# Kernel optimization log

Measured on AMD Instinct MI355X. Metric: run time of the kernel, lower is better.

The kernel has to match this reference:

```python
import jax, jax.numpy as jnp
import numpy as np

N_NODES = 200000
N_EDGES = 200000
X_SIZE = 256
H_SIZE = 256


def setup_inputs() -> dict:
    key = jax.random.key(0)
    ks = jax.random.split(key, 8)
    s = 1.0 / np.sqrt(H_SIZE)
    return {
        "x": jax.random.normal(ks[0], (N_NODES, X_SIZE), jnp.float32),
        "h": jax.random.normal(ks[1], (N_NODES, H_SIZE), jnp.float32),
        "c": jax.random.normal(ks[2], (N_NODES, H_SIZE), jnp.float32),
        "W_iou": jax.random.normal(ks[3], (3 * H_SIZE, X_SIZE), jnp.float32) * s,
        "U_iou": jax.random.normal(ks[4], (3 * H_SIZE, H_SIZE), jnp.float32) * s,
        "b_iou": jnp.zeros((1, 3 * H_SIZE), jnp.float32),
        "U_f_w": jax.random.normal(ks[5], (H_SIZE, H_SIZE), jnp.float32) * s,
        "U_f_b": jnp.zeros((H_SIZE,), jnp.float32),
        "edge_src": jax.random.randint(ks[6], (N_EDGES,), 0, N_NODES, jnp.int32),
        "edge_dst": jax.random.randint(ks[7], (N_EDGES,), 0, N_NODES, jnp.int32),
    }


def reference(x, h, c, W_iou, U_iou, b_iou, U_f_w, U_f_b, edge_src, edge_dst):
    n = x.shape[0]
    # --- message + reduce (DGL mailbox flattened to edge list) ---
    h_child = h[edge_src]                                   # [E, H] gather
    c_child = c[edge_src]                                   # [E, H]
    f = jax.nn.sigmoid(h_child @ U_f_w.T + U_f_b)           # per-child forget gate
    h_tild = jax.ops.segment_sum(h_child, edge_dst, num_segments=n)      # sum_j h_j
    c_agg = jax.ops.segment_sum(f * c_child, edge_dst, num_segments=n)   # sum_j f_j*c_j
    # --- node iou: W_iou(x) (node data) + U_iou(h_tild) from reduce ---
    iou = x @ W_iou.T + h_tild @ U_iou.T + b_iou            # [N, 3H]
    # --- apply_node_func ---
    i, o, u = jnp.split(iou, 3, axis=1)
    i = jax.nn.sigmoid(i)
    o = jax.nn.sigmoid(o)
    u = jnp.tanh(u)
    c_new = i * u + c_agg
    h_new = o * jnp.tanh(c_new)
    return h_new, c_new
```

## Files before the change

kernel.cpp:

```cpp
#include <hip/hip_runtime.h>

#define NN 200000
#define NE 200000
#define HD 256

typedef __attribute__((ext_vector_type(8))) short short8;
typedef __attribute__((ext_vector_type(4))) short short4v;
typedef __attribute__((ext_vector_type(4))) float f32x4;
typedef __attribute__((ext_vector_type(4))) unsigned int u32x4;

static __device__ __forceinline__ unsigned short f2bf(float f) {
  unsigned u = __float_as_uint(f);
  u = (u + 0x7FFFu + ((u >> 16) & 1u)) >> 16;
  return (unsigned short)u;
}
static __device__ __forceinline__ float bf2f(unsigned short u) {
  return __uint_as_float(((unsigned)u) << 16);
}
static __device__ __forceinline__ float sigmoidf_(float x) {
  return 1.0f / (1.0f + __expf(-x));
}
static __device__ __forceinline__ float tanhf_(float x) {
  return 2.0f / (1.0f + __expf(-2.0f * x)) - 1.0f;
}
static __device__ __forceinline__ void atomAddF(float* p, float v) {
  __hip_atomic_fetch_add(p, v, __ATOMIC_RELAXED, __HIP_MEMORY_SCOPE_AGENT);
}
static __device__ __forceinline__ int atomAddI(int* p, int v) {
  return __hip_atomic_fetch_add(p, v, __ATOMIC_RELAXED, __HIP_MEMORY_SCOPE_AGENT);
}

#if defined(__HIP_DEVICE_COMPILE__)
static __device__ __forceinline__ void gload_lds16(const void* g, void* l) {
  __builtin_amdgcn_global_load_lds(
      (const __attribute__((address_space(1))) void*)g,
      (__attribute__((address_space(3))) void*)l, 16, 0, 0);
}
static __device__ __forceinline__ unsigned pack_hi16(unsigned lo, unsigned hi) {
  return __builtin_amdgcn_perm(hi, lo, 0x07060302u);
}
#else
static __device__ __forceinline__ void gload_lds16(const void*, void*) {}
static __device__ __forceinline__ unsigned pack_hi16(unsigned lo, unsigned hi) {
  return (lo >> 16) | (hi & 0xffff0000u);
}
#endif

#define OFF_WFB    0u
#define OFF_BP     131072u
#define OFF_BPERM  917504u
#define OFF_ROWPTR 920576u
#define OFF_NEXT   1720832u
#define OFF_SLOT   2520832u
#define OFF_PSRC   3320832u
#define OFF_BSUM   4120832u
#define OFF_ZERO   4121856u
#define OFF_FC     4122880u
#define WS_NEED    106522880ull

__global__ __launch_bounds__(256) void prep_kernel(
    const float* __restrict__ Ufw, const float* __restrict__ Wiou,
    const float* __restrict__ Uiou, const float* __restrict__ biou,
    unsigned short* __restrict__ Wfb, unsigned short* __restrict__ Bp,
    float* __restrict__ bperm) {
  int idx = blockIdx.x * 256 + threadIdx.x;
  if (idx < 65536) {
    Wfb[idx] = f2bf(Ufw[idx]);
  } else if (idx < 458752) {
    int o = idx - 65536;
    int kc = o / 24576;
    int rem = o - kc * 24576;
    int tt = rem / 512;
    int rem2 = rem - tt * 512;
    int ln = rem2 >> 3, e = rem2 & 7;
    int cc = ln & 15, kgp = ln >> 4;
    int kk = kc * 32 + kgp * 8 + e;
    int g = tt % 3, tj = tt / 3;
    int orow = g * 256 + tj * 16 + cc;
    float v = (kk < 256) ? Wiou[orow * 256 + kk] : Uiou[orow * 256 + (kk - 256)];
    Bp[o] = f2bf(v);
  } else if (idx < 459520) {
    int j2 = idx - 458752;
    int T = j2 >> 4, cc = j2 & 15;
    int g = T % 3, tj = T / 3;
    bperm[j2] = biou[g * 256 + tj * 16 + cc];
  }
}

__global__ __launch_bounds__(256) void prep_fb_kernel(
    const float* __restrict__ Ufw, const float* __restrict__ Wiou,
    const float* __restrict__ Uiou, const float* __restrict__ biou,
    unsigned short* __restrict__ Wfb, unsigned short* __restrict__ Wioub,
    unsigned short* __restrict__ Uioub, float* __restrict__ bperm) {
  int idx = blockIdx.x * 256 + threadIdx.x;
  if (idx < 65536) {
    Wfb[idx] = f2bf(Ufw[idx]);
  } else if (idx < 262144) {
    int i2 = idx - 65536;
    int rp = i2 >> 8, k = i2 & 255;
    int T = rp >> 4, cc = rp & 15;
    int g = T % 3, tj = T / 3;
    Wioub[i2] = f2bf(Wiou[(g * 256 + tj * 16 + cc) * 256 + k]);
  } else if (idx < 458752) {
    int i2 = idx - 262144;
    int rp = i2 >> 8, k = i2 & 255;
    int T = rp >> 4, cc = rp & 15;
    int g = T % 3, tj = T / 3;
    Uioub[i2] = f2bf(Uiou[(g * 256 + tj * 16 + cc) * 256 + k]);
  } else if (idx < 459520) {
    int j2 = idx - 458752;
    int T = j2 >> 4, cc = j2 & 15;
    int g = T % 3, tj = T / 3;
    bperm[j2] = biou[g * 256 + tj * 16 + cc];
  }
}

__global__ __launch_bounds__(256) void hist_kernel(const int* __restrict__ edst,
                                                   int* __restrict__ cnt) {
  int e = blockIdx.x * 256 + threadIdx.x;
  if (e < NE) atomAddI(&cnt[edst[e]], 1);
}

__global__ __launch_bounds__(256) void scan_part(const int* __restrict__ cnt,
                                                 int* __restrict__ rp,
                                                 int* __restrict__ bsum) {
  __shared__ int sd[256];
  int t = threadIdx.x;
  int base = blockIdx.x * 1024 + t * 4;
  int v0 = (base + 0 < NN) ? cnt[base + 0] : 0;
  int v1 = (base + 1 < NN) ? cnt[base + 1] : 0;
  int v2 = (base + 2 < NN) ? cnt[base + 2] : 0;
  int v3 = (base + 3 < NN) ? cnt[base + 3] : 0;
  int s = v0 + v1 + v2 + v3;
  sd[t] = s;
  __syncthreads();
  for (int off = 1; off < 256; off <<= 1) {
    int add = (t >= off) ? sd[t - off] : 0;
    __syncthreads();
    sd[t] += add;
    __syncthreads();
  }
  int run = sd[t] - s;
  if (base + 0 < NN) rp[base + 0] = run; run += v0;
  if (base + 1 < NN) rp[base + 1] = run; run += v1;
  if (base + 2 < NN) rp[base + 2] = run; run += v2;
  if (base + 3 < NN) rp[base + 3] = run;
  if (t == 255) bsum[blockIdx.x] = sd[255];
}

__global__ __launch_bounds__(256) void scan_top(int* __restrict__ bsum,
                                                int* __restrict__ rp, int nb) {
  __shared__ int sd[256];
  int t = threadIdx.x;
  int v = (t < nb) ? bsum[t] : 0;
  sd[t] = v;
  __syncthreads();
  for (int off = 1; off < 256; off <<= 1) {
    int add = (t >= off) ? sd[t - off] : 0;
    __syncthreads();
    sd[t] += add;
    __syncthreads();
  }
  bsum[t] = sd[t] - v;
  if (t == 0) rp[NN] = NE;
}

__global__ __launch_bounds__(256) void scan_add(int* __restrict__ rp,
                                                const int* __restrict__ bsum,
                                                int* __restrict__ nxt) {
  int t = threadIdx.x;
  int base = blockIdx.x * 1024 + t * 4;
  int off = bsum[blockIdx.x];
#pragma unroll
  for (int j = 0; j < 4; ++j) {
    int i = base + j;
    if (i < NN) {
      int val = rp[i] + off;
      rp[i] = val;
      nxt[i] = val;
    }
  }
}

__global__ __launch_bounds__(256) void scatter_kernel(
    const int* __restrict__ esrc, const int* __restrict__ edst,
    int* __restrict__ nxt, int* __restrict__ slotArr, int* __restrict__ psrc) {
  int e = blockIdx.x * 256 + threadIdx.x;
  if (e < NE) {
    int d = edst[e];
    int pos = atomAddI(&nxt[d], 1);
    slotArr[e] = pos;
    psrc[pos] = esrc[e];
  }
}

#define F_AS 72
#define F_BS 72

__global__ __launch_bounds__(256) void edge_fc_kernel(
    const float* __restrict__ h, const float* __restrict__ c,
    const unsigned short* __restrict__ Wfb, const float* __restrict__ Ufb,
    const int* __restrict__ esrc, const int* __restrict__ slotArr,
    unsigned short* __restrict__ fcb) {
  __shared__ __align__(16) unsigned short Als[64 * F_AS];
  __shared__ __align__(16) unsigned short Bls[256 * F_BS];
  __shared__ int srcl[64], slotl[64];

  const int tid = threadIdx.x;
  const int e0 = blockIdx.x * 64;
  if (tid < 64) { srcl[tid] = esrc[e0 + tid]; slotl[tid] = slotArr[e0 + tid]; }
  __syncthreads();

  const int lane = tid & 63;
  const int wv = tid >> 6;
  const int wm = wv >> 1, wn = wv & 1;
  const int cbase = lane & 15;
  const int kg = lane >> 4;

  f32x4 acc[2][8];
#pragma unroll
  for (int i = 0; i < 2; ++i)
#pragma unroll
    for (int j = 0; j < 8; ++j) acc[i][j] = {0.f, 0.f, 0.f, 0.f};

  const int arow = tid >> 2;
  const int acg = tid & 3;
  const float* hrow = h + (size_t)srcl[arow] * HD;

  for (int kc = 0; kc < 4; ++kc) {
    const int k0 = kc * 64;
    const float4* s4 = (const float4*)(hrow + k0 + acg * 16);
    float4 q0 = s4[0], q1 = s4[1], q2 = s4[2], q3 = s4[3];
    short8 p0, p1;
    p0[0] = f2bf(q0.x); p0[1] = f2bf(q0.y); p0[2] = f2bf(q0.z); p0[3] = f2bf(q0.w);
    p0[4] = f2bf(q1.x); p0[5] = f2bf(q1.y); p0[6] = f2bf(q1.z); p0[7] = f2bf(q1.w);
    p1[0] = f2bf(q2.x); p1[1] = f2bf(q2.y); p1[2] = f2bf(q2.z); p1[3] = f2bf(q2.w);
    p1[4] = f2bf(q3.x); p1[5] = f2bf(q3.y); p1[6] = f2bf(q3.z); p1[7] = f2bf(q3.w);
    short8* ap = (short8*)&Als[arow * F_AS + acg * 16];
    ap[0] = p0; ap[1] = p1;
#pragma unroll
    for (int i = 0; i < 8; ++i) {
      int f = tid + 256 * i;
      int row = f >> 3, ch = f & 7;
      short8 vb = *(const short8*)(Wfb + row * 256 + k0 + ch * 8);
      *(short8*)&Bls[row * F_BS + ch * 8] = vb;
    }
    __syncthreads();
#pragma unroll
    for (int ks = 0; ks < 2; ++ks) {
      short8 a0 = *(const short8*)&Als[(wm * 32 + cbase) * F_AS + ks * 32 + kg * 8];
      short8 a1 = *(const short8*)&Als[(wm * 32 + 16 + cbase) * F_AS + ks * 32 + kg * 8];
#pragma unroll
      for (int nt = 0; nt < 8; ++nt) {
        short8 b = *(const short8*)&Bls[(wn * 128 + nt * 16 + cbase) * F_BS + ks * 32 + kg * 8];
        acc[0][nt] = __builtin_amdgcn_mfma_f32_16x16x32_bf16(a0, b, acc[0][nt], 0, 0, 0);
        acc[1][nt] = __builtin_amdgcn_mfma_f32_16x16x32_bf16(a1, b, acc[1][nt], 0, 0, 0);
      }
    }
    __syncthreads();
  }
  const int rsub = kg * 4;
#pragma unroll
  for (int nt = 0; nt < 8; ++nt) {
    const int coln = wn * 128 + nt * 16 + cbase;
    const float bias = Ufb[coln];
#pragma unroll
    for (int mt = 0; mt < 2; ++mt) {
#pragma unroll
      for (int j = 0; j < 4; ++j) {
        const int el = wm * 32 + mt * 16 + rsub + j;
        const float fg = sigmoidf_(acc[mt][nt][j] + bias);
        const float cv = c[(size_t)srcl[el] * HD + coln];
        fcb[(size_t)slotl[el] * HD + coln] = f2bf(fg * cv);
      }
    }
  }
}

__global__ __launch_bounds__(256) void gather_kernel(
    const float* __restrict__ h, const int* __restrict__ rp,
    const int* __restrict__ psrc, unsigned short* __restrict__ fcb,
    float* __restrict__ cagg) {
  const int tid = threadIdx.x;
  const int node = blockIdx.x * 32 + (tid >> 3);
  const int cg = tid & 7;
  const int s0 = rp[node], s1 = rp[node + 1];

  float hs[32], cs[32];
#pragma unroll
  for (int q = 0; q < 32; ++q) { hs[q] = 0.f; cs[q] = 0.f; }

  for (int s = s0; s < s1; ++s) {
    const int src = psrc[s];
    const float4* hp = (const float4*)(h + (size_t)src * HD + cg * 32);
    const short8* fp = (const short8*)(fcb + (size_t)s * HD + cg * 32);
#pragma unroll
    for (int q = 0; q < 8; ++q) {
      float4 v = hp[q];
      hs[4 * q + 0] += v.x; hs[4 * q + 1] += v.y;
      hs[4 * q + 2] += v.z; hs[4 * q + 3] += v.w;
    }
#pragma unroll
    for (int q = 0; q < 4; ++q) {
      short8 w = fp[q];
#pragma unroll
      for (int e = 0; e < 8; ++e) cs[8 * q + e] += bf2f((unsigned short)w[e]);
    }
  }
  float4* cp = (float4*)(cagg + (size_t)node * HD + cg * 32);
#pragma unroll
  for (int q = 0; q < 8; ++q) {
    float4 v = {cs[4 * q + 0], cs[4 * q + 1], cs[4 * q + 2], cs[4 * q + 3]};
    cp[q] = v;
  }
  if (s1 > s0) {
    short8* hd = (short8*)(fcb + (size_t)s0 * HD + cg * 32);
#pragma unroll
    for (int q = 0; q < 4; ++q) {
      short8 p;
#pragma unroll
      for (int e = 0; e < 8; ++e) p[e] = f2bf(hs[8 * q + e]);
      hd[q] = p;
    }
  }
}

__global__ __launch_bounds__(256, 3) void iou_gemm5_kernel(
    const float* __restrict__ x, const unsigned short* __restrict__ Bp,
    const float* __restrict__ bperm, const int* __restrict__ rp,
    const unsigned short* __restrict__ fcb, const char* __restrict__ zpage,
    float* __restrict__ out) {
  __shared__ __align__(16) unsigned char Als[32768];
  __shared__ __align__(16) unsigned char Bls[12288];

  const int tid = threadIdx.x;
  const int lane = tid & 63;
  const int wv = tid >> 6;
  const int cbase = lane & 15;
  const int kg = lane >> 4;

  const int bid = blockIdx.x;
  const int cg = bid & 7;
  const int r0 = (bid >> 3) * 128;
  const bool full = (r0 + 128 <= NN);

  const unsigned xswz = ((unsigned)(tid & 15) * 16) ^ ((((unsigned)(tid >> 4)) & 7) << 5);
  const char* xbase = (const char*)x + (size_t)(full ? (r0 + (tid >> 4)) : (NN - 1)) * 1024 + xswz;

  const unsigned hswz = ((unsigned)(tid & 7) * 16) ^ ((((unsigned)(tid >> 3)) & 7) << 4);
  const char* hsrc[4];
#pragma unroll
  for (int i = 0; i < 4; ++i) {
    int rr = r0 + i * 32 + (tid >> 3);
    if (rr >= NN) rr = NN - 1;
    const int s0 = rp[rr], s1 = rp[rr + 1];
    const char* base = (s1 > s0) ? (const char*)(fcb + (size_t)s0 * HD) : zpage;
    hsrc[i] = base + hswz;
  }

  f32x4 acc[2][6];
#pragma unroll
  for (int m = 0; m < 2; ++m)
#pragma unroll
    for (int t = 0; t < 6; ++t) acc[m][t] = {0.f, 0.f, 0.f, 0.f};

  const int frow0 = wv * 32 + cbase;
  const unsigned swx = ((unsigned)(frow0 & 7)) << 5;
  const unsigned swh = ((unsigned)(frow0 & 7)) << 4;
  const unsigned char* ar0x = Als + frow0 * 256;
  const unsigned char* ar1x = Als + (frow0 + 16) * 256;
  const unsigned char* ar0h = Als + frow0 * 128;
  const unsigned char* ar1h = Als + (frow0 + 16) * 128;
  unsigned char* lA = Als + wv * 1024 + lane * 16;
  unsigned char* lB = Bls + wv * 1024 + lane * 16;
  const unsigned char* bread = Bls + lane * 16;

  for (int kc = 0; kc < 4; ++kc) {
#pragma unroll
    for (int i = 0; i < 3; ++i) {
      const int f = i * 4 + wv;
      const int kch = f / 6, t = f - kch * 6;
      gload_lds16((const char*)Bp + ((size_t)(kc * 2 + kch) * 48 + cg * 6 + t) * 1024 + lane * 16,
                  lB + i * 4096);
    }
    if (full) {
#pragma unroll
      for (int i = 0; i < 8; ++i)
        gload_lds16(xbase + (size_t)i * 16384 + kc * 256, lA + i * 4096);
    } else {
#pragma unroll
      for (int i = 0; i < 8; ++i) {
        int rr = r0 + i * 16 + (tid >> 4);
        if (rr >= NN) rr = NN - 1;
        gload_lds16((const char*)x + (size_t)rr * 1024 + kc * 256 + xswz, lA + i * 4096);
      }
    }
    __syncthreads();
#pragma unroll
    for (int ks = 0; ks < 2; ++ks) {
      u32x4 q0 = *(const u32x4*)(ar0x + ((unsigned)(ks * 128 + kg * 32) ^ swx));
      u32x4 q1 = *(const u32x4*)(ar0x + ((unsigned)(ks * 128 + kg * 32 + 16) ^ swx));
      u32x4 q2 = *(const u32x4*)(ar1x + ((unsigned)(ks * 128 + kg * 32) ^ swx));
      u32x4 q3 = *(const u32x4*)(ar1x + ((unsigned)(ks * 128 + kg * 32 + 16) ^ swx));
      u32x4 p0, p1;
      p0[0] = pack_hi16(q0[0], q0[1]); p0[1] = pack_hi16(q0[2], q0[3]);
      p0[2] = pack_hi16(q1[0], q1[1]); p0[3] = pack_hi16(q1[2], q1[3]);
      p1[0] = pack_hi16(q2[0], q2[1]); p1[1] = pack_hi16(q2[2], q2[3]);
      p1[2] = pack_hi16(q3[0], q3[1]); p1[3] = pack_hi16(q3[2], q3[3]);
      short8 a0 = __builtin_bit_cast(short8, p0);
      short8 a1 = __builtin_bit_cast(short8, p1);
#pragma unroll
      for (int t = 0; t < 6; ++t) {
        short8 b = *(const short8*)(bread + (ks * 6 + t) * 1024);
        acc[0][t] = __builtin_amdgcn_mfma_f32_16x16x32_bf16(a0, b, acc[0][t], 0, 0, 0);
        acc[1][t] = __builtin_amdgcn_mfma_f32_16x16x32_bf16(a1, b, acc[1][t], 0, 0, 0);
      }
    }
    __syncthreads();
  }

  for (int kc = 4; kc < 8; ++kc) {
#pragma unroll
    for (int i = 0; i < 3; ++i) {
      const int f = i * 4 + wv;
      const int kch = f / 6, t = f - kch * 6;
      gload_lds16((const char*)Bp + ((size_t)(kc * 2 + kch) * 48 + cg * 6 + t) * 1024 + lane * 16,
                  lB + i * 4096);
    }
    const int kcH = kc - 4;
#pragma unroll
    for (int i = 0; i < 4; ++i)
      gload_lds16(hsrc[i] + kcH * 128, lA + i * 4096);
    __syncthreads();
#pragma unroll
    for (int ks = 0; ks < 2; ++ks) {
      short8 a0 = *(const short8*)(ar0h + ((unsigned)(ks * 64 + kg * 16) ^ swh));
      short8 a1 = *(const short8*)(ar1h + ((unsigned)(ks * 64 + kg * 16) ^ swh));
#pragma unroll
      for (int t = 0; t < 6; ++t) {
        short8 b = *(const short8*)(bread + (ks * 6 + t) * 1024);
        acc[0][t] = __builtin_amdgcn_mfma_f32_16x16x32_bf16(a0, b, acc[0][t], 0, 0, 0);
        acc[1][t] = __builtin_amdgcn_mfma_f32_16x16x32_bf16(a1, b, acc[1][t], 0, 0, 0);
      }
    }
    __syncthreads();
  }

  float* outc = out + (size_t)NN * HD;
#pragma unroll
  for (int t3 = 0; t3 < 2; ++t3) {
    const int TT = cg * 6 + 3 * t3;
    const float bi = bperm[(TT + 0) * 16 + cbase];
    const float bo = bperm[(TT + 1) * 16 + cbase];
    const float bu = bperm[(TT + 2) * 16 + cbase];
    const int j = (cg * 2 + t3) * 16 + cbase;
#pragma unroll
    for (int mf = 0; mf < 2; ++mf) {
#pragma unroll
      for (int jr = 0; jr < 4; ++jr) {
        const int gr = r0 + wv * 32 + mf * 16 + kg * 4 + jr;
        if (gr < NN) {
          const size_t idx = (size_t)gr * HD + j;
          const float iv = sigmoidf_(acc[mf][3 * t3 + 0][jr] + bi);
          const float ov = sigmoidf_(acc[mf][3 * t3 + 1][jr] + bo);
          const float uv = tanhf_(acc[mf][3 * t3 + 2][jr] + bu);
          const float cn = iv * uv + outc[idx];
          out[idx] = ov * tanhf_(cn);
          outc[idx] = cn;
        }
      }
    }
  }
}

__global__ __launch_bounds__(256) void edge_kernel(
    const float* __restrict__ h, const float* __restrict__ c,
    const unsigned short* __restrict__ Wfb, const float* __restrict__ Ufb,
    const int* __restrict__ esrc, const int* __restrict__ edst,
    float* h_tild, float* c_agg) {
  __shared__ __align__(16) unsigned short Als[64 * F_AS];
  __shared__ __align__(16) unsigned short Bls[256 * F_BS];
  __shared__ int srcl[64], dstl[64];

  const int tid = threadIdx.x;
  const int e0 = blockIdx.x * 64;
  if (tid < 64) { srcl[tid] = esrc[e0 + tid]; dstl[tid] = edst[e0 + tid]; }
  __syncthreads();

  const int lane = tid & 63;
  const int wv = tid >> 6;
  const int wm = wv >> 1, wn = wv & 1;
  const int cbase = lane & 15;
  const int kg = lane >> 4;

  f32x4 acc[2][8];
#pragma unroll
  for (int i = 0; i < 2; ++i)
#pragma unroll
    for (int j = 0; j < 8; ++j) acc[i][j] = {0.f, 0.f, 0.f, 0.f};

  const int arow = tid >> 2;
  const int acg = tid & 3;
  const float* hrow = h + (size_t)srcl[arow] * HD;
  float* htrow = h_tild + (size_t)dstl[arow] * HD;

  for (int kc = 0; kc < 4; ++kc) {
    const int k0 = kc * 64;
    const float4* s4 = (const float4*)(hrow + k0 + acg * 16);
    float4 q0 = s4[0], q1 = s4[1], q2 = s4[2], q3 = s4[3];
    short8 p0, p1;
    p0[0] = f2bf(q0.x); p0[1] = f2bf(q0.y); p0[2] = f2bf(q0.z); p0[3] = f2bf(q0.w);
    p0[4] = f2bf(q1.x); p0[5] = f2bf(q1.y); p0[6] = f2bf(q1.z); p0[7] = f2bf(q1.w);
    p1[0] = f2bf(q2.x); p1[1] = f2bf(q2.y); p1[2] = f2bf(q2.z); p1[3] = f2bf(q2.w);
    p1[4] = f2bf(q3.x); p1[5] = f2bf(q3.y); p1[6] = f2bf(q3.z); p1[7] = f2bf(q3.w);
    short8* ap = (short8*)&Als[arow * F_AS + acg * 16];
    ap[0] = p0; ap[1] = p1;
    {
      float* hp = htrow + k0 + acg * 16;
      atomAddF(hp + 0, q0.x);  atomAddF(hp + 1, q0.y);
      atomAddF(hp + 2, q0.z);  atomAddF(hp + 3, q0.w);
      atomAddF(hp + 4, q1.x);  atomAddF(hp + 5, q1.y);
      atomAddF(hp + 6, q1.z);  atomAddF(hp + 7, q1.w);
      atomAddF(hp + 8, q2.x);  atomAddF(hp + 9, q2.y);
      atomAddF(hp + 10, q2.z); atomAddF(hp + 11, q2.w);
      atomAddF(hp + 12, q3.x); atomAddF(hp + 13, q3.y);
      atomAddF(hp + 14, q3.z); atomAddF(hp + 15, q3.w);
    }
#pragma unroll
    for (int i = 0; i < 8; ++i) {
      int f = tid + 256 * i;
      int row = f >> 3, ch = f & 7;
      short8 vb = *(const short8*)(Wfb + row * 256 + k0 + ch * 8);
      *(short8*)&Bls[row * F_BS + ch * 8] = vb;
    }
    __syncthreads();
#pragma unroll
    for (int ks = 0; ks < 2; ++ks) {
      short8 a0 = *(const short8*)&Als[(wm * 32 + cbase) * F_AS + ks * 32 + kg * 8];
      short8 a1 = *(const short8*)&Als[(wm * 32 + 16 + cbase) * F_AS + ks * 32 + kg * 8];
#pragma unroll
      for (int nt = 0; nt < 8; ++nt) {
        short8 b = *(const short8*)&Bls[(wn * 128 + nt * 16 + cbase) * F_BS + ks * 32 + kg * 8];
        acc[0][nt] = __builtin_amdgcn_mfma_f32_16x16x32_bf16(a0, b, acc[0][nt], 0, 0, 0);
        acc[1][nt] = __builtin_amdgcn_mfma_f32_16x16x32_bf16(a1, b, acc[1][nt], 0, 0, 0);
      }
    }
    __syncthreads();
  }
  const int rsub = kg * 4;
#pragma unroll
  for (int nt = 0; nt < 8; ++nt) {
    const int coln = wn * 128 + nt * 16 + cbase;
    const float bias = Ufb[coln];
#pragma unroll
    for (int mt = 0; mt < 2; ++mt) {
#pragma unroll
      for (int j = 0; j < 4; ++j) {
        const int el = wm * 32 + mt * 16 + rsub + j;
        const float fg = sigmoidf_(acc[mt][nt][j] + bias);
        const float cv = c[(size_t)srcl[el] * HD + coln];
        atomAddF(c_agg + (size_t)dstl[el] * HD + coln, fg * cv);
      }
    }
  }
}

#define I_AS 40
#define I_BS 40

__global__ __launch_bounds__(256) void iou_kernel(
    const float* __restrict__ x, const unsigned short* __restrict__ Wioub,
    const unsigned short* __restrict__ Uioub, const float* __restrict__ bperm,
    float* out) {
  __shared__ __align__(16) unsigned short Als[32 * I_AS];
  __shared__ __align__(16) unsigned short Bls[768 * I_BS];

  const int tid = threadIdx.x;
  const int lane = tid & 63;
  const int wv = tid >> 6;
  const int wm = wv >> 1, wn = wv & 1;
  const int cbase = lane & 15;
  const int kg = lane >> 4;
  const int r0 = blockIdx.x * 32;

  float* h_tild = out;
  float* c_agg = out + (size_t)NN * HD;

  f32x4 acc[24];
#pragma unroll
  for (int t = 0; t < 24; ++t) acc[t] = {0.f, 0.f, 0.f, 0.f};

  const int arow = tid >> 3;
  const int acg = tid & 7;

  for (int pass = 0; pass < 2; ++pass) {
    const float* As = pass ? h_tild : x;
    const unsigned short* Bs = pass ? Uioub : Wioub;
    for (int kc = 0; kc < 8; ++kc) {
      const int k0 = kc * 32;
      float4 q = *(const float4*)(As + (size_t)(r0 + arow) * HD + k0 + acg * 4);
      short4v p;
      p[0] = f2bf(q.x); p[1] = f2bf(q.y); p[2] = f2bf(q.z); p[3] = f2bf(q.w);
      *(short4v*)&Als[arow * I_AS + acg * 4] = p;
#pragma unroll
      for (int i = 0; i < 12; ++i) {
        int f = tid + 256 * i;
        int row = f >> 2, ch = f & 3;
        short8 vb = *(const short8*)(Bs + row * 256 + k0 + ch * 8);
        *(short8*)&Bls[row * I_BS + ch * 8] = vb;
      }
      __syncthreads();
      short8 a = *(const short8*)&Als[(wm * 16 + cbase) * I_AS + kg * 8];
#pragma unroll
      for (int tt = 0; tt < 24; ++tt) {
        short8 b = *(const short8*)&Bls[((wn * 24 + tt) * 16 + cbase) * I_BS + kg * 8];
        acc[tt] = __builtin_amdgcn_mfma_f32_16x16x32_bf16(a, b, acc[tt], 0, 0, 0);
      }
      __syncthreads();
    }
  }
  const int rsub = kg * 4;
#pragma unroll
  for (int t3 = 0; t3 < 8; ++t3) {
    const int T = wn * 24 + 3 * t3;
    const float bi = bperm[(T + 0) * 16 + cbase];
    const float bo = bperm[(T + 1) * 16 + cbase];
    const float bu = bperm[(T + 2) * 16 + cbase];
    const int j = (wn * 8 + t3) * 16 + cbase;
#pragma unroll
    for (int jr = 0; jr < 4; ++jr) {
      const int r = r0 + wm * 16 + rsub + jr;
      const size_t idx = (size_t)r * HD + j;
      const float iv = sigmoidf_(acc[3 * t3 + 0][jr] + bi);
      const float ov = sigmoidf_(acc[3 * t3 + 1][jr] + bo);
      const float uv = tanhf_(acc[3 * t3 + 2][jr] + bu);
      const float cn = iv * uv + c_agg[idx];
      out[idx] = ov * tanhf_(cn);
      c_agg[idx] = cn;
    }
  }
}

extern "C" void kernel_launch(void* const* d_in, const int* in_sizes, int n_in,
                              void* d_out, int out_size, void* d_ws, size_t ws_size,
                              hipStream_t stream) {
  const float* x    = (const float*)d_in[0];
  const float* h    = (const float*)d_in[1];
  const float* c    = (const float*)d_in[2];
  const float* Wiou = (const float*)d_in[3];
  const float* Uiou = (const float*)d_in[4];
  const float* biou = (const float*)d_in[5];
  const float* Ufw  = (const float*)d_in[6];
  const float* Ufb  = (const float*)d_in[7];
  const int* esrc   = (const int*)d_in[8];
  const int* edst   = (const int*)d_in[9];
  float* out = (float*)d_out;

  char* ws = (char*)d_ws;
  unsigned short* Wfb   = (unsigned short*)(ws + OFF_WFB);
  unsigned short* Bp    = (unsigned short*)(ws + OFF_BP);
  float* bperm          = (float*)(ws + OFF_BPERM);

  if (ws_size >= WS_NEED) {
    int* rpp  = (int*)(ws + OFF_ROWPTR);
    int* nxt  = (int*)(ws + OFF_NEXT);
    int* slot = (int*)(ws + OFF_SLOT);
    int* psrc = (int*)(ws + OFF_PSRC);
    int* bsum = (int*)(ws + OFF_BSUM);
    char* zpage = ws + OFF_ZERO;
    unsigned short* fcb = (unsigned short*)(ws + OFF_FC);

    (void)hipMemsetAsync(nxt, 0, (size_t)NN * sizeof(int), stream);
    (void)hipMemsetAsync(zpage, 0, 1024, stream);
    prep_kernel<<<1795, 256, 0, stream>>>(Ufw, Wiou, Uiou, biou, Wfb, Bp, bperm);
    hist_kernel<<<(NE + 255) / 256, 256, 0, stream>>>(edst, nxt);
    scan_part<<<(NN + 1023) / 1024, 256, 0, stream>>>(nxt, rpp, bsum);
    scan_top<<<1, 256, 0, stream>>>(bsum, rpp, (NN + 1023) / 1024);
    scan_add<<<(NN + 1023) / 1024, 256, 0, stream>>>(rpp, bsum, nxt);
    scatter_kernel<<<(NE + 255) / 256, 256, 0, stream>>>(esrc, edst, nxt, slot, psrc);
    edge_fc_kernel<<<NE / 64, 256, 0, stream>>>(h, c, Wfb, Ufb, esrc, slot, fcb);
    gather_kernel<<<NN / 32, 256, 0, stream>>>(h, rpp, psrc, fcb, out + (size_t)NN * HD);
    const int rgrps = (NN + 127) / 128;
    iou_gemm5_kernel<<<rgrps * 8, 256, 0, stream>>>(x, Bp, bperm, rpp, fcb, zpage, out);
  } else {
    unsigned short* Wioub = (unsigned short*)(ws + OFF_BP);
    unsigned short* Uioub = (unsigned short*)(ws + OFF_BP + 393216);
    (void)hipMemsetAsync(d_out, 0, (size_t)out_size * sizeof(float), stream);
    prep_fb_kernel<<<1795, 256, 0, stream>>>(Ufw, Wiou, Uiou, biou, Wfb, Wioub, Uioub, bperm);
    edge_kernel<<<NE / 64, 256, 0, stream>>>(h, c, Wfb, Ufb, esrc, edst,
                                             out, out + (size_t)NN * HD);
    iou_kernel<<<NN / 32, 256, 0, stream>>>(x, Wioub, Uioub, bperm, out);
  }
}
```

Measured before the change: 835.2 us.

## Pre-convert x to bf16 once and use a leaner iou GEMM kernel

```diff
diff --git a/kernel.cpp b/kernel.cpp
--- a/kernel.cpp
+++ b/kernel.cpp
@@ -57,6 +57,8 @@
 #define OFF_ZERO   4121856u
 #define OFF_FC     4122880u
 #define WS_NEED    106522880ull
+#define OFF_XB     106522880ull
+#define WS_NEED2   208922880ull
 
 __global__ __launch_bounds__(256) void prep_kernel(
     const float* __restrict__ Ufw, const float* __restrict__ Wiou,
@@ -87,6 +89,19 @@
   }
 }
 
+__global__ __launch_bounds__(256) void xcvt_kernel(const float* __restrict__ x,
+                                                   unsigned short* __restrict__ xb) {
+  const size_t i = ((size_t)blockIdx.x * 256 + threadIdx.x) * 8;
+  if (i < (size_t)NN * HD) {
+    float4 a = *(const float4*)(x + i);
+    float4 b = *(const float4*)(x + i + 4);
+    short8 p;
+    p[0] = f2bf(a.x); p[1] = f2bf(a.y); p[2] = f2bf(a.z); p[3] = f2bf(a.w);
+    p[4] = f2bf(b.x); p[5] = f2bf(b.y); p[6] = f2bf(b.z); p[7] = f2bf(b.w);
+    *(short8*)(xb + i) = p;
+  }
+}
+
 __global__ __launch_bounds__(256) void prep_fb_kernel(
     const float* __restrict__ Ufw, const float* __restrict__ Wiou,
     const float* __restrict__ Uiou, const float* __restrict__ biou,
@@ -325,6 +340,110 @@
   }
 }
 
+__global__ __launch_bounds__(256, 4) void iou_gemm6_kernel(
+    const unsigned short* __restrict__ xb, const unsigned short* __restrict__ Bp,
+    const float* __restrict__ bperm, const int* __restrict__ rp,
+    const unsigned short* __restrict__ fcb, const char* __restrict__ zpage,
+    float* __restrict__ out) {
+  __shared__ __align__(16) unsigned char Als[16384];
+  __shared__ __align__(16) unsigned char Bls[12288];
+
+  const int tid = threadIdx.x;
+  const int lane = tid & 63;
+  const int wv = tid >> 6;
+  const int cbase = lane & 15;
+  const int kg = lane >> 4;
+
+  const int bid = blockIdx.x;
+  const int cg = bid & 7;
+  const int r0 = (bid >> 3) * 128;
+
+  const unsigned hswz = ((unsigned)(tid & 7) * 16) ^ ((((unsigned)(tid >> 3)) & 7) << 4);
+  const char* xsrc[4];
+  const char* hsrc[4];
+#pragma unroll
+  for (int i = 0; i < 4; ++i) {
+    int rr = r0 + i * 32 + (tid >> 3);
+    if (rr >= NN) rr = NN - 1;
+    xsrc[i] = (const char*)xb + (size_t)rr * 512 + hswz;
+    const int s0 = rp[rr], s1 = rp[rr + 1];
+    const char* base = (s1 > s0) ? (const char*)(fcb + (size_t)s0 * HD) : zpage;
+    hsrc[i] = base + hswz;
+  }
+
+  f32x4 acc[2][6];
+#pragma unroll
+  for (int m = 0; m < 2; ++m)
+#pragma unroll
+    for (int t = 0; t < 6; ++t) acc[m][t] = {0.f, 0.f, 0.f, 0.f};
+
+  const int frow0 = wv * 32 + cbase;
+  const unsigned swh = ((unsigned)(frow0 & 7)) << 4;
+  const unsigned char* ar0 = Als + frow0 * 128;
+  const unsigned char* ar1 = Als + (frow0 + 16) * 128;
+  unsigned char* lA = Als + wv * 1024 + lane * 16;
+  unsigned char* lB = Bls + wv * 1024 + lane * 16;
+  const unsigned char* bread = Bls + lane * 16;
+
+  for (int kc = 0; kc < 8; ++kc) {
+#pragma unroll
+    for (int i = 0; i < 3; ++i) {
+      const int f = i * 4 + wv;
+      const int kch = f / 6, t = f - kch * 6;
+      gload_lds16((const char*)Bp + ((size_t)(kc * 2 + kch) * 48 + cg * 6 + t) * 1024 + lane * 16,
+                  lB + i * 4096);
+    }
+    if (kc < 4) {
+      const int ko = kc * 128;
+#pragma unroll
+      for (int i = 0; i < 4; ++i) gload_lds16(xsrc[i] + ko, lA + i * 4096);
+    } else {
+      const int ko = (kc - 4) * 128;
+#pragma unroll
+      for (int i = 0; i < 4; ++i) gload_lds16(hsrc[i] + ko, lA + i * 4096);
+    }
+    __syncthreads();
+#pragma unroll
+    for (int ks = 0; ks < 2; ++ks) {
+      short8 a0 = *(const short8*)(ar0 + ((unsigned)(ks * 64 + kg * 16) ^ swh));
+      short8 a1 = *(const short8*)(ar1 + ((unsigned)(ks * 64 + kg * 16) ^ swh));
+#pragma unroll
+      for (int t = 0; t < 6; ++t) {
+        short8 b = *(const short8*)(bread + (ks * 6 + t) * 1024);
+        acc[0][t] = __builtin_amdgcn_mfma_f32_16x16x32_bf16(a0, b, acc[0][t], 0, 0, 0);
+        acc[1][t] = __builtin_amdgcn_mfma_f32_16x16x32_bf16(a1, b, acc[1][t], 0, 0, 0);
+      }
+    }
+    __syncthreads();
+  }
+
+  float* outc = out + (size_t)NN * HD;
+#pragma unroll
+  for (int t3 = 0; t3 < 2; ++t3) {
+    const int TT = cg * 6 + 3 * t3;
+    const float bi = bperm[(TT + 0) * 16 + cbase];
+    const float bo = bperm[(TT + 1) * 16 + cbase];
+    const float bu = bperm[(TT + 2) * 16 + cbase];
+    const int j = (cg * 2 + t3) * 16 + cbase;
+#pragma unroll
+    for (int mf = 0; mf < 2; ++mf) {
+#pragma unroll
+      for (int jr = 0; jr < 4; ++jr) {
+        const int gr = r0 + wv * 32 + mf * 16 + kg * 4 + jr;
+        if (gr < NN) {
+          const size_t idx = (size_t)gr * HD + j;
+          const float iv = sigmoidf_(acc[mf][3 * t3 + 0][jr] + bi);
+          const float ov = sigmoidf_(acc[mf][3 * t3 + 1][jr] + bo);
+          const float uv = tanhf_(acc[mf][3 * t3 + 2][jr] + bu);
+          const float cn = iv * uv + outc[idx];
+          out[idx] = ov * tanhf_(cn);
+          outc[idx] = cn;
+        }
+      }
+    }
+  }
+}
+
 __global__ __launch_bounds__(256, 3) void iou_gemm5_kernel(
     const float* __restrict__ x, const unsigned short* __restrict__ Bp,
     const float* __restrict__ bperm, const int* __restrict__ rp,
@@ -681,7 +800,13 @@
     edge_fc_kernel<<<NE / 64, 256, 0, stream>>>(h, c, Wfb, Ufb, esrc, slot, fcb);
     gather_kernel<<<NN / 32, 256, 0, stream>>>(h, rpp, psrc, fcb, out + (size_t)NN * HD);
     const int rgrps = (NN + 127) / 128;
-    iou_gemm5_kernel<<<rgrps * 8, 256, 0, stream>>>(x, Bp, bperm, rpp, fcb, zpage, out);
+    if (ws_size >= WS_NEED2) {
+      unsigned short* xb = (unsigned short*)(ws + OFF_XB);
+      xcvt_kernel<<<(int)(((size_t)NN * HD / 8 + 255) / 256), 256, 0, stream>>>(x, xb);
+      iou_gemm6_kernel<<<rgrps * 8, 256, 0, stream>>>(xb, Bp, bperm, rpp, fcb, zpage, out);
+    } else {
+      iou_gemm5_kernel<<<rgrps * 8, 256, 0, stream>>>(x, Bp, bperm, rpp, fcb, zpage, out);
+    }
   } else {
     unsigned short* Wioub = (unsigned short*)(ws + OFF_BP);
     unsigned short* Uioub = (unsigned short*)(ws + OFF_BP + 393216);
```

Result: faster. 797.2 us (-4.6%).
